# Performance work log

Measured on AMD Instinct MI355X. Metric: run time of the kernel, lower is better.

The kernel has to match this reference:

```python
import jax, jax.numpy as jnp
import numpy as np

B, S, D = 2, 2048, 1024
H, DH = 16, 64
EPS = 1e-5

def setup_inputs() -> dict:
    key = jax.random.key(0)
    ks = jax.random.split(key, 8)
    s = 0.02
    return {
        "x": jax.random.normal(ks[0], (B, S, D), dtype=jnp.float32),
        "ln_gamma": jnp.ones((D,), jnp.float32),
        "ln_beta": jnp.zeros((D,), jnp.float32),
        "wq": jax.random.normal(ks[1], (D, H * DH), jnp.float32) * s,
        "bq": jnp.zeros((H * DH,), jnp.float32),
        "wk": jax.random.normal(ks[2], (D, H * DH), jnp.float32) * s,
        "bk": jnp.zeros((H * DH,), jnp.float32),
        "wv": jax.random.normal(ks[3], (D, H * DH), jnp.float32) * s,
        "bv": jnp.zeros((H * DH,), jnp.float32),
        "wo": jax.random.normal(ks[4], (H * DH, D), jnp.float32) * s,
        "bo": jnp.zeros((D,), jnp.float32),
    }

def reference(x, ln_gamma, ln_beta, wq, bq, wk, bk, wv, bv, wo, bo):
    # Pre-LayerNorm over d_model
    mu = jnp.mean(x, axis=-1, keepdims=True)
    var = jnp.var(x, axis=-1, keepdims=True)
    xn = (x - mu) * jax.lax.rsqrt(var + EPS) * ln_gamma + ln_beta

    b, s, _ = xn.shape
    q = (xn @ wq + bq).reshape(b, s, H, DH)
    k = (xn @ wk + bk).reshape(b, s, H, DH)
    v = (xn @ wv + bv).reshape(b, s, H, DH)

    scale = jnp.sqrt(jnp.float32(DH))
    scores = jnp.einsum('bihd,bjhd->bhij', q, k) / scale  # [b,h,s,s]
    att = jax.nn.softmax(scores, axis=-1)
    out = jnp.einsum('bhij,bjhd->bihd', att, v).reshape(b, s, H * DH)
    return out @ wo + bo
```

## Files before the change

kernel.cpp:

```cpp
#include <hip/hip_runtime.h>
#include <math.h>

#define SEQ   2048
#define DM    1024
#define NHEAD 16
#define HD    64
#define NTOK  4096
#define EPS   1e-5f
#define SCALE_C 0.18033688f

typedef __attribute__((ext_vector_type(8))) short v8s;
typedef __attribute__((ext_vector_type(4))) short v4s;
typedef __attribute__((ext_vector_type(4))) float v4f;
typedef unsigned short ushort_t;

#define GLOAD16(g, l) __builtin_amdgcn_global_load_lds( \
    (const __attribute__((address_space(1))) unsigned int*)(g), \
    (__attribute__((address_space(3))) unsigned int*)(l), 16, 0, 0)

#if defined(__has_builtin)
#if __has_builtin(__builtin_amdgcn_mfma_f32_16x16x16_bf16)
#define MFMA16(va, vb, vc) __builtin_amdgcn_mfma_f32_16x16x16_bf16(va, vb, vc, 0, 0, 0)
#elif __has_builtin(__builtin_amdgcn_mfma_f32_16x16x16bf16_1k)
#define MFMA16(va, vb, vc) __builtin_amdgcn_mfma_f32_16x16x16bf16_1k(va, vb, vc, 0, 0, 0)
#endif
#endif
#ifndef MFMA16
__device__ __forceinline__ v4f mfma16_asm(v4s a, v4s b, v4f c) {
  asm volatile("s_nop 2\n\tv_mfma_f32_16x16x16_bf16 %0, %1, %2, %0\n\ts_nop 4"
               : "+v"(c) : "v"(a), "v"(b));
  return c;
}
#define MFMA16(va, vb, vc) mfma16_asm(va, vb, vc)
#endif

__device__ __forceinline__ unsigned short f2bf(float f) {
  union { float f; unsigned u; } v; v.f = f;
  unsigned r = v.u + 0x7FFFu + ((v.u >> 16) & 1u);
  return (unsigned short)(r >> 16);
}

__device__ __forceinline__ unsigned pack2_bf16(float a, float b) {
  union { float f; unsigned u; } ua, ub;
  ua.f = a; ub.f = b;
  return __builtin_amdgcn_perm(ub.u + 0x8000u, ua.u + 0x8000u, 0x07060302u);
}

__global__ __launch_bounds__(256) void prep_kernel(
    const float* __restrict__ x, const float* __restrict__ g,
    const float* __restrict__ be, ushort_t* __restrict__ y,
    const float* __restrict__ w0, const float* __restrict__ w1,
    const float* __restrict__ w2, const float* __restrict__ w3,
    ushort_t* __restrict__ o0, ushort_t* __restrict__ o1,
    ushort_t* __restrict__ o2, ushort_t* __restrict__ o3) {
  __shared__ float red[8];
  __shared__ float mu_s, rs_s;
  __shared__ float tile[64][65];
  const int t = threadIdx.x;
  if (blockIdx.x < NTOK) {
    const int row = blockIdx.x;
    const float4 v = ((const float4*)(x + (size_t)row * DM))[t];
    float s  = v.x + v.y + v.z + v.w;
    float ss = v.x*v.x + v.y*v.y + v.z*v.z + v.w*v.w;
    #pragma unroll
    for (int off = 32; off > 0; off >>= 1) {
      s  += __shfl_down(s,  off, 64);
      ss += __shfl_down(ss, off, 64);
    }
    const int wid = t >> 6, lane = t & 63;
    if (lane == 0) { red[wid] = s; red[4 + wid] = ss; }
    __syncthreads();
    if (t == 0) {
      const float S  = red[0] + red[1] + red[2] + red[3];
      const float SS = red[4] + red[5] + red[6] + red[7];
      const float mu  = S * (1.0f / DM);
      const float var = SS * (1.0f / DM) - mu * mu;
      mu_s = mu; rs_s = rsqrtf(var + EPS);
    }
    __syncthreads();
    const float mu = mu_s, r = rs_s;
    const float4 gv = ((const float4*)g)[t];
    const float4 bv = ((const float4*)be)[t];
    ushort4 o;
    o.x = f2bf((v.x - mu) * r * gv.x + bv.x);
    o.y = f2bf((v.y - mu) * r * gv.y + bv.y);
    o.z = f2bf((v.z - mu) * r * gv.z + bv.z);
    o.w = f2bf((v.w - mu) * r * gv.w + bv.w);
    *(ushort4*)(y + (size_t)row * DM + t * 4) = o;
  } else {
    const int i = blockIdx.x - NTOK;
    const int z = i >> 8;
    const float* w = (z==0) ? w0 : (z==1) ? w1 : (z==2) ? w2 : w3;
    ushort_t* o    = (z==0) ? o0 : (z==1) ? o1 : (z==2) ? o2 : o3;
    const int n0 = (i & 15) * 64, k0 = ((i >> 4) & 15) * 64;
    const int r = t >> 4, c4 = (t & 15) * 4;
    #pragma unroll
    for (int ii = 0; ii < 4; ++ii) {
      const float4 v = *(const float4*)(w + (size_t)(k0 + r + ii*16) * DM + n0 + c4);
      tile[r + ii*16][c4 + 0] = v.x;
      tile[r + ii*16][c4 + 1] = v.y;
      tile[r + ii*16][c4 + 2] = v.z;
      tile[r + ii*16][c4 + 3] = v.w;
    }
    __syncthreads();
    #pragma unroll
    for (int ii = 0; ii < 4; ++ii) {
      const int n = r + ii*16;
      ushort4 o4;
      o4.x = f2bf(tile[c4 + 0][n]);
      o4.y = f2bf(tile[c4 + 1][n]);
      o4.z = f2bf(tile[c4 + 2][n]);
      o4.w = f2bf(tile[c4 + 3][n]);
      *(ushort4*)(o + (size_t)(n0 + n) * DM + k0 + c4) = o4;
    }
  }
}

__device__ __forceinline__ void gemm_main(ushort_t* lsa, ushort_t* lsb,
    const ushort_t* A, const ushort_t* WT, int m0, int n0, v4f acc[4][4]) {
  const int tid = threadIdx.x;
  const int wid = tid >> 6, lane = tid & 63;
  const int mh = (wid & 1) << 6, nh = (wid >> 1) << 6;
  const int r16 = lane & 15, quad = lane >> 4;
  const int srow = lane >> 2, sch = lane & 3;
  for (int k0 = 0; k0 < DM; k0 += 64) {
    __syncthreads();
    #pragma unroll
    for (int s = 0; s < 2; ++s) {
      #pragma unroll
      for (int j = 0; j < 2; ++j) {
        const int o = wid * 2 + j;
        GLOAD16(A  + (size_t)(m0 + o*16 + srow) * DM + k0 + s*32 + sch*8, lsa + s*4096 + o*512);
        GLOAD16(WT + (size_t)(n0 + o*16 + srow) * DM + k0 + s*32 + sch*8, lsb + s*4096 + o*512);
      }
    }
    __syncthreads();
    #pragma unroll
    for (int s = 0; s < 2; ++s) {
      v8s af[4], bfr[4];
      #pragma unroll
      for (int i = 0; i < 4; ++i) {
        af[i]  = *(const v8s*)(lsa + s*4096 + (mh + i*16 + r16)*32 + quad*8);
        bfr[i] = *(const v8s*)(lsb + s*4096 + (nh + i*16 + r16)*32 + quad*8);
      }
      #pragma unroll
      for (int i = 0; i < 4; ++i)
        #pragma unroll
        for (int j = 0; j < 4; ++j)
          acc[i][j] = __builtin_amdgcn_mfma_f32_16x16x32_bf16(af[i], bfr[j], acc[i][j], 0, 0, 0);
    }
  }
}

__global__ __launch_bounds__(256, 2) void gemm_qkv(const ushort_t* __restrict__ xn,
    const ushort_t* __restrict__ wtq, const ushort_t* __restrict__ wtk, const ushort_t* __restrict__ wtv,
    const float* __restrict__ bq, const float* __restrict__ bk, const float* __restrict__ bv,
    ushort_t* __restrict__ qo, ushort_t* __restrict__ ko, ushort_t* __restrict__ vto) {
  __shared__ ushort_t lsa[128*64];
  __shared__ ushort_t lsb[128*64];
  const int z = blockIdx.z;
  const ushort_t* WT = (z == 0) ? wtq : (z == 1) ? wtk : wtv;
  const float* bias  = (z == 0) ? bq  : (z == 1) ? bk  : bv;
  const int m0 = blockIdx.y * 128, n0 = blockIdx.x * 128;
  v4f acc[4][4];
  #pragma unroll
  for (int i = 0; i < 4; ++i)
    #pragma unroll
    for (int j = 0; j < 4; ++j) acc[i][j] = (v4f){0.f, 0.f, 0.f, 0.f};
  gemm_main(lsa, lsb, xn, WT, m0, n0, acc);
  const int tid = threadIdx.x, wid = tid >> 6, lane = tid & 63;
  const int mh = (wid & 1) << 6, nh = (wid >> 1) << 6;
  const int r16 = lane & 15, quad = lane >> 4;
  if (z < 2) {
    ushort_t* out = (z == 0) ? qo : ko;
    const float sc = (z == 0) ? SCALE_C : 1.0f;
    #pragma unroll
    for (int bn = 0; bn < 4; ++bn) {
      const int col = n0 + nh + bn*16 + r16;
      const float bb = bias[col];
      #pragma unroll
      for (int am = 0; am < 4; ++am) {
        const int tb = m0 + mh + am*16 + quad*4;
        #pragma unroll
        for (int r = 0; r < 4; ++r)
          out[(size_t)(tb + r) * DM + col] = f2bf((acc[am][bn][r] + bb) * sc);
      }
    }
  } else {
    #pragma unroll
    for (int bn = 0; bn < 4; ++bn) {
      const int col = n0 + nh + bn*16 + r16;
      const float bb = bias[col];
      const int h = col >> 6, d = col & 63;
      #pragma unroll
      for (int am = 0; am < 4; ++am) {
        const int tb = m0 + mh + am*16 + quad*4;
        const int b = tb >> 11, t = tb & 2047;
        const int bh = b * NHEAD + h;
        ushort4 o4;
        o4.x = f2bf(acc[am][bn][0] + bb);
        o4.y = f2bf(acc[am][bn][1] + bb);
        o4.z = f2bf(acc[am][bn][2] + bb);
        o4.w = f2bf(acc[am][bn][3] + bb);
        const size_t idx = (size_t)bh * 131072 + (size_t)(t >> 6) * 4096 +
                           (size_t)((((t >> 4) & 3) * 4) + (d >> 4)) * 256 +
                           ((t >> 2) & 3) * 64 + (d & 15) * 4;
        *(ushort4*)(vto + idx) = o4;
      }
    }
  }
}

__global__ __launch_bounds__(256, 2) void gemm_out(const ushort_t* __restrict__ A,
    const ushort_t* __restrict__ WT, const float* __restrict__ bias,
    float* __restrict__ out) {
  __shared__ ushort_t lsa[128*64];
  __shared__ ushort_t lsb[128*64];
  const int m0 = blockIdx.y * 128, n0 = blockIdx.x * 128;
  v4f acc[4][4];
  #pragma unroll
  for (int i = 0; i < 4; ++i)
    #pragma unroll
    for (int j = 0; j < 4; ++j) acc[i][j] = (v4f){0.f, 0.f, 0.f, 0.f};
  gemm_main(lsa, lsb, A, WT, m0, n0, acc);
  const int tid = threadIdx.x, wid = tid >> 6, lane = tid & 63;
  const int mh = (wid & 1) << 6, nh = (wid >> 1) << 6;
  const int r16 = lane & 15, quad = lane >> 4;
  #pragma unroll
  for (int bn = 0; bn < 4; ++bn) {
    const int col = n0 + nh + bn*16 + r16;
    const float bb = bias[col];
    #pragma unroll
    for (int am = 0; am < 4; ++am) {
      const int tb = m0 + mh + am*16 + quad*4;
      #pragma unroll
      for (int r = 0; r < 4; ++r)
        out[(size_t)(tb + r) * DM + col] = acc[am][bn][r] + bb;
    }
  }
}

#define OHALF ((size_t)32 * 2048 * 64)
#define LHALF (32 * 2048)
template<int SPLIT>
__global__ __launch_bounds__(256, 8) void attn_kernel(
    const ushort_t* __restrict__ Q, const ushort_t* __restrict__ K,
    const ushort_t* __restrict__ Vt, ushort_t* __restrict__ O,
    float* __restrict__ Opart, float* __restrict__ lpart) {
  __shared__ ushort_t kbuf[8*512];
  __shared__ ushort_t vbuf[8*512];
  const int tid = threadIdx.x, wid = tid >> 6, lane = tid & 63;
  const int r16 = lane & 15, quad = lane >> 4;
  const int q0 = blockIdx.x * 64, bh = blockIdx.y;
  const int half = SPLIT ? blockIdx.z : 0;
  const int b = bh >> 4, h = bh & 15;
  const ushort_t* gQ = Q + (size_t)b * SEQ * DM + h * HD;
  const ushort_t* gK = K + (size_t)b * SEQ * DM + h * HD;
  const ushort_t* gV = Vt + (size_t)bh * 131072;

  const int qtok = q0 + wid * 16 + r16;
  const v8s qf0 = *(const v8s*)(gQ + (size_t)qtok * DM + quad * 8);
  const v8s qf1 = *(const v8s*)(gQ + (size_t)qtok * DM + 32 + quad * 8);
  v4f acco[4];
  #pragma unroll
  for (int i = 0; i < 4; ++i) acco[i] = (v4f){0.f, 0.f, 0.f, 0.f};
  float lrun = 0.f;

  const int NIT = SPLIT ? (SEQ / 128) : (SEQ / 64);
  const int kt0 = half * NIT;
  const int o0 = wid * 2, o1 = wid * 2 + 1;
  const ushort_t* srcK0 = gK + (size_t)((o0 >> 1) * 16 + r16) * DM + (o0 & 1) * 32 + quad * 8;
  const ushort_t* srcK1 = gK + (size_t)((o1 >> 1) * 16 + r16) * DM + (o1 & 1) * 32 + quad * 8;
  const ushort_t* srcV  = gV + lane * 8;

  {
    const int k0 = kt0 * 64;
    GLOAD16(srcK0 + (size_t)k0 * DM, kbuf + o0 * 512);
    GLOAD16(srcK1 + (size_t)k0 * DM, kbuf + o1 * 512);
    GLOAD16(srcV + (size_t)kt0 * 4096 + o0 * 512, vbuf + o0 * 512);
    GLOAD16(srcV + (size_t)kt0 * 4096 + o1 * 512, vbuf + o1 * 512);
  }
  __syncthreads();

  for (int it = 0; it < NIT; ++it) {
    const int kt = kt0 + it;
    uint4 rk0, rk1, rv0, rv1;
    const bool pf = (it + 1 < NIT);
    if (pf) {
      const size_t k0n = (size_t)(kt + 1) * 64;
      rk0 = *(const uint4*)(srcK0 + k0n * DM);
      rk1 = *(const uint4*)(srcK1 + k0n * DM);
      rv0 = *(const uint4*)(srcV + (size_t)(kt + 1) * 4096 + o0 * 512);
      rv1 = *(const uint4*)(srcV + (size_t)(kt + 1) * 4096 + o1 * 512);
    }

    v4f sacc[4];
    #pragma unroll
    for (int g = 0; g < 4; ++g) sacc[g] = (v4f){0.f, 0.f, 0.f, 0.f};
    #pragma unroll
    for (int g = 0; g < 4; ++g) {
      const v8s ka0 = *(const v8s*)(kbuf + (g*2 + 0) * 512 + lane * 8);
      const v8s ka1 = *(const v8s*)(kbuf + (g*2 + 1) * 512 + lane * 8);
      sacc[g] = __builtin_amdgcn_mfma_f32_16x16x32_bf16(ka0, qf0, sacc[g], 0, 0, 0);
      sacc[g] = __builtin_amdgcn_mfma_f32_16x16x32_bf16(ka1, qf1, sacc[g], 0, 0, 0);
    }

    float ls = 0.f;
    v4s pfrag[4];
    #pragma unroll
    for (int g = 0; g < 4; ++g) {
      float e0 = __builtin_amdgcn_exp2f(sacc[g][0]);
      float e1 = __builtin_amdgcn_exp2f(sacc[g][1]);
      float e2 = __builtin_amdgcn_exp2f(sacc[g][2]);
      float e3 = __builtin_amdgcn_exp2f(sacc[g][3]);
      ls += (e0 + e1) + (e2 + e3);
      union { v4s s; uint2 u; } pk;
      pk.u.x = pack2_bf16(e0, e1);
      pk.u.y = pack2_bf16(e2, e3);
      pfrag[g] = pk.s;
    }
    ls += __shfl_xor(ls, 16, 64);
    ls += __shfl_xor(ls, 32, 64);
    lrun += ls;

    #pragma unroll
    for (int dg = 0; dg < 4; ++dg) {
      #pragma unroll
      for (int g = 0; g < 4; ++g) {
        const v4s vf = *(const v4s*)(vbuf + (g*4 + dg) * 256 + quad * 64 + r16 * 4);
        acco[dg] = MFMA16(vf, pfrag[g], acco[dg]);
      }
    }

    __syncthreads();
    if (pf) {
      *(uint4*)(kbuf + o0 * 512 + lane * 8) = rk0;
      *(uint4*)(kbuf + o1 * 512 + lane * 8) = rk1;
      *(uint4*)(vbuf + o0 * 512 + lane * 8) = rv0;
      *(uint4*)(vbuf + o1 * 512 + lane * 8) = rv1;
    }
    __syncthreads();
  }

  if (SPLIT) {
    float* Op = Opart + half * OHALF + ((size_t)bh * SEQ + qtok) * 64;
    #pragma unroll
    for (int dg = 0; dg < 4; ++dg)
      *(v4f*)(Op + dg*16 + quad*4) = acco[dg];
    if (quad == 0) lpart[half * LHALF + bh * SEQ + qtok] = lrun;
  } else {
    const float inv = 1.f / lrun;
    ushort_t* gO = O + (size_t)b * SEQ * DM + h * HD;
    #pragma unroll
    for (int dg = 0; dg < 4; ++dg) {
      ushort4 o4;
      o4.x = f2bf(acco[dg][0] * inv);
      o4.y = f2bf(acco[dg][1] * inv);
      o4.z = f2bf(acco[dg][2] * inv);
      o4.w = f2bf(acco[dg][3] * inv);
      *(ushort4*)(gO + (size_t)qtok * DM + dg*16 + quad*4) = o4;
    }
  }
}

__global__ __launch_bounds__(256) void combine_kernel(
    const float* __restrict__ Opart, const float* __restrict__ lpart,
    ushort_t* __restrict__ ob) {
  const int tok = blockIdx.x;
  const int b = tok >> 11, t = tok & 2047;
  const int dm0 = threadIdx.x * 4;
  const int h = dm0 >> 6, d = dm0 & 63;
  const int bh = b * NHEAD + h;
  const size_t idx = ((size_t)bh * SEQ + t) * 64 + d;
  const float4 a = *(const float4*)(Opart + idx);
  const float4 c = *(const float4*)(Opart + OHALF + idx);
  const float l = lpart[bh * SEQ + t] + lpart[LHALF + bh * SEQ + t];
  const float inv = 1.f / l;
  ushort4 o4;
  o4.x = f2bf((a.x + c.x) * inv);
  o4.y = f2bf((a.y + c.y) * inv);
  o4.z = f2bf((a.z + c.z) * inv);
  o4.w = f2bf((a.w + c.w) * inv);
  *(ushort4*)(ob + (size_t)tok * DM + dm0) = o4;
}

extern "C" void kernel_launch(void* const* d_in, const int* in_sizes, int n_in,
                              void* d_out, int out_size, void* d_ws, size_t ws_size,
                              hipStream_t stream) {
  const float* x     = (const float*)d_in[0];
  const float* gamma = (const float*)d_in[1];
  const float* beta  = (const float*)d_in[2];
  const float* wq    = (const float*)d_in[3];
  const float* bq    = (const float*)d_in[4];
  const float* wk    = (const float*)d_in[5];
  const float* bk    = (const float*)d_in[6];
  const float* wv    = (const float*)d_in[7];
  const float* bv    = (const float*)d_in[8];
  const float* wo    = (const float*)d_in[9];
  const float* bo    = (const float*)d_in[10];
  float* out = (float*)d_out;

  unsigned char* w8 = (unsigned char*)d_ws;
  const size_t MB = 1024 * 1024;
  ushort_t* xn  = (ushort_t*)(w8 + 0 * MB);
  ushort_t* qb  = (ushort_t*)(w8 + 8 * MB);
  ushort_t* kb  = (ushort_t*)(w8 + 16 * MB);
  ushort_t* vt  = (ushort_t*)(w8 + 24 * MB);
  ushort_t* wtq = (ushort_t*)(w8 + 32 * MB);
  ushort_t* wtk = (ushort_t*)(w8 + 34 * MB);
  ushort_t* wtv = (ushort_t*)(w8 + 36 * MB);
  ushort_t* wto = (ushort_t*)(w8 + 38 * MB);
  float* Opart  = (float*)(w8 + 40 * MB);
  float* lpart  = (float*)(w8 + 72 * MB);
  ushort_t* ob  = xn;

  prep_kernel<<<dim3(NTOK + 1024), dim3(256), 0, stream>>>(
      x, gamma, beta, xn, wq, wk, wv, wo, wtq, wtk, wtv, wto);
  gemm_qkv<<<dim3(8, 32, 3), dim3(256), 0, stream>>>(xn, wtq, wtk, wtv, bq, bk, bv, qb, kb, vt);
  if (ws_size >= 73 * MB) {
    attn_kernel<1><<<dim3(SEQ / 64, 2 * NHEAD, 2), dim3(256), 0, stream>>>(
        qb, kb, vt, nullptr, Opart, lpart);
    combine_kernel<<<dim3(NTOK), dim3(256), 0, stream>>>(Opart, lpart, ob);
  } else {
    attn_kernel<0><<<dim3(SEQ / 64, 2 * NHEAD, 1), dim3(256), 0, stream>>>(
        qb, kb, vt, ob, nullptr, nullptr);
  }
  gemm_out<<<dim3(8, 32, 1), dim3(256), 0, stream>>>(ob, wto, bo, out);
}
```

Baseline: 212.8 us.

## Swizzle GEMM block order across XCDs and shrink out-proj tile to 128x64

Both GEMM kernels now run on a flat 1D grid whose block index is remapped so that consecutive hardware-dispatched blocks, which are spread round-robin over the XCDs, land on tiles that share operand panels within each XCD's L2. The output projection switches from 128x128 tiles (256 blocks) to 128x64 tiles (512 blocks) with its own inline K loop. This gives better wave coverage on 256 CUs. The smaller tile lowers per-block data reuse and adds extra A-panel reads in exchange for higher occupancy.

Result: faster. 207.2 us (-2.7%).

```diff
diff --git a/kernel.cpp b/kernel.cpp
--- a/kernel.cpp
+++ b/kernel.cpp
@@ -158,10 +158,14 @@
     ushort_t* __restrict__ qo, ushort_t* __restrict__ ko, ushort_t* __restrict__ vto) {
   __shared__ ushort_t lsa[128*64];
   __shared__ ushort_t lsb[128*64];
-  const int z = blockIdx.z;
-  const ushort_t* WT = (z == 0) ? wtq : (z == 1) ? wtk : wtv;
-  const float* bias  = (z == 0) ? bq  : (z == 1) ? bk  : bv;
-  const int m0 = blockIdx.y * 128, n0 = blockIdx.x * 128;
+  const int flat = blockIdx.x;
+  const int nf = (flat & 7) * 96 + (flat >> 3);
+  const int zi = nf >> 8;
+  const int yi = (nf >> 3) & 31;
+  const int xi = nf & 7;
+  const ushort_t* WT = (zi == 0) ? wtq : (zi == 1) ? wtk : wtv;
+  const float* bias  = (zi == 0) ? bq  : (zi == 1) ? bk  : bv;
+  const int m0 = yi * 128, n0 = xi * 128;
   v4f acc[4][4];
   #pragma unroll
   for (int i = 0; i < 4; ++i)
@@ -171,9 +175,9 @@
   const int tid = threadIdx.x, wid = tid >> 6, lane = tid & 63;
   const int mh = (wid & 1) << 6, nh = (wid >> 1) << 6;
   const int r16 = lane & 15, quad = lane >> 4;
-  if (z < 2) {
-    ushort_t* out = (z == 0) ? qo : ko;
-    const float sc = (z == 0) ? SCALE_C : 1.0f;
+  if (zi < 2) {
+    ushort_t* out = (zi == 0) ? qo : ko;
+    const float sc = (zi == 0) ? SCALE_C : 1.0f;
     #pragma unroll
     for (int bn = 0; bn < 4; ++bn) {
       const int col = n0 + nh + bn*16 + r16;
@@ -215,19 +219,50 @@
     const ushort_t* __restrict__ WT, const float* __restrict__ bias,
     float* __restrict__ out) {
   __shared__ ushort_t lsa[128*64];
-  __shared__ ushort_t lsb[128*64];
-  const int m0 = blockIdx.y * 128, n0 = blockIdx.x * 128;
-  v4f acc[4][4];
+  __shared__ ushort_t lsb[64*64];
+  const int flat = blockIdx.x;
+  const int nf = (flat & 7) * 64 + (flat >> 3);
+  const int n0 = (nf & 15) * 64, m0 = (nf >> 4) * 128;
+  const int tid = threadIdx.x;
+  const int wid = tid >> 6, lane = tid & 63;
+  const int mh = (wid & 1) << 6, nh = (wid >> 1) << 5;
+  const int r16 = lane & 15, quad = lane >> 4;
+  const int srow = lane >> 2, sch = lane & 3;
+  v4f acc[4][2];
   #pragma unroll
   for (int i = 0; i < 4; ++i)
     #pragma unroll
-    for (int j = 0; j < 4; ++j) acc[i][j] = (v4f){0.f, 0.f, 0.f, 0.f};
-  gemm_main(lsa, lsb, A, WT, m0, n0, acc);
-  const int tid = threadIdx.x, wid = tid >> 6, lane = tid & 63;
-  const int mh = (wid & 1) << 6, nh = (wid >> 1) << 6;
-  const int r16 = lane & 15, quad = lane >> 4;
+    for (int j = 0; j < 2; ++j) acc[i][j] = (v4f){0.f, 0.f, 0.f, 0.f};
+  for (int k0 = 0; k0 < DM; k0 += 64) {
+    __syncthreads();
+    #pragma unroll
+    for (int s = 0; s < 2; ++s) {
+      #pragma unroll
+      for (int j = 0; j < 2; ++j) {
+        const int o = wid * 2 + j;
+        GLOAD16(A + (size_t)(m0 + o*16 + srow) * DM + k0 + s*32 + sch*8, lsa + s*4096 + o*512);
+      }
+      GLOAD16(WT + (size_t)(n0 + wid*16 + srow) * DM + k0 + s*32 + sch*8, lsb + s*2048 + wid*512);
+    }
+    __syncthreads();
+    #pragma unroll
+    for (int s = 0; s < 2; ++s) {
+      v8s af[4], bfr[2];
+      #pragma unroll
+      for (int i = 0; i < 4; ++i)
+        af[i] = *(const v8s*)(lsa + s*4096 + (mh + i*16 + r16)*32 + quad*8);
+      #pragma unroll
+      for (int j = 0; j < 2; ++j)
+        bfr[j] = *(const v8s*)(lsb + s*2048 + (nh + j*16 + r16)*32 + quad*8);
+      #pragma unroll
+      for (int i = 0; i < 4; ++i)
+        #pragma unroll
+        for (int j = 0; j < 2; ++j)
+          acc[i][j] = __builtin_amdgcn_mfma_f32_16x16x32_bf16(af[i], bfr[j], acc[i][j], 0, 0, 0);
+    }
+  }
   #pragma unroll
-  for (int bn = 0; bn < 4; ++bn) {
+  for (int bn = 0; bn < 2; ++bn) {
     const int col = n0 + nh + bn*16 + r16;
     const float bb = bias[col];
     #pragma unroll
@@ -416,7 +451,7 @@
 
   prep_kernel<<<dim3(NTOK + 1024), dim3(256), 0, stream>>>(
       x, gamma, beta, xn, wq, wk, wv, wo, wtq, wtk, wtv, wto);
-  gemm_qkv<<<dim3(8, 32, 3), dim3(256), 0, stream>>>(xn, wtq, wtk, wtv, bq, bk, bv, qb, kb, vt);
+  gemm_qkv<<<dim3(768), dim3(256), 0, stream>>>(xn, wtq, wtk, wtv, bq, bk, bv, qb, kb, vt);
   if (ws_size >= 73 * MB) {
     attn_kernel<1><<<dim3(SEQ / 64, 2 * NHEAD, 2), dim3(256), 0, stream>>>(
         qb, kb, vt, nullptr, Opart, lpart);
@@ -425,5 +460,5 @@
     attn_kernel<0><<<dim3(SEQ / 64, 2 * NHEAD, 1), dim3(256), 0, stream>>>(
         qb, kb, vt, ob, nullptr, nullptr);
   }
-  gemm_out<<<dim3(8, 32, 1), dim3(256), 0, stream>>>(ob, wto, bo, out);
-}
+  gemm_out<<<dim3(512), dim3(256), 0, stream>>>(ob, wto, bo, out);
+}
```
